# Performance work log

Hardware: AMD Instinct MI355X
Metric: run time of the kernel (lower is better)

## Reference

```python
import jax, jax.numpy as jnp
import numpy as np

B, N, D = 4, 2048, 1024
DF = 4 * D
EPS = 1e-5


def _layernorm(x, w, b):
    mu = jnp.mean(x, axis=-1, keepdims=True)
    var = jnp.mean(jnp.square(x - mu), axis=-1, keepdims=True)
    return (x - mu) * jax.lax.rsqrt(var + EPS) * w + b


def setup_inputs() -> dict:
    key = jax.random.key(0)
    ks = jax.random.split(key, 8)
    x = jax.random.normal(ks[0], (B, N, D), dtype=jnp.float32)
    # conv filter param (torch init is zeros; use small randn for numeric coverage)
    weights = jax.random.normal(ks[1], (1, 1, N), dtype=jnp.float32) * 0.02
    # registered buffer: sqrt(1/(i+1)) per token, shape (1, N, 1)
    scale = jnp.sqrt(1.0 / (jnp.arange(N, dtype=jnp.float32) + 1.0))[None, :, None]
    ln1_w = jnp.ones((D,), jnp.float32)
    ln1_b = jnp.zeros((D,), jnp.float32)
    W1 = jax.random.normal(ks[2], (DF, D), dtype=jnp.float32) * 0.02
    b1 = jnp.zeros((DF,), jnp.float32)
    W2 = jax.random.normal(ks[3], (D, DF), dtype=jnp.float32) * 0.02
    b2 = jnp.zeros((D,), jnp.float32)
    scalar = jax.random.normal(ks[4], (1,), dtype=jnp.float32) * 0.1
    ln2_w = jnp.ones((D,), jnp.float32)
    ln2_b = jnp.zeros((D,), jnp.float32)
    return dict(x=x, weights=weights, scale=scale, ln1_w=ln1_w, ln1_b=ln1_b,
                W1=W1, b1=b1, W2=W2, b2=b2, scalar=scalar, ln2_w=ln2_w, ln2_b=ln2_b)


def reference(x, weights, scale, ln1_w, ln1_b, W1, b1, W2, b2, scalar, ln2_w, ln2_b):
    n = weights.shape[-1]
    # FFT token-mixing conv: operate over token axis. x: (B,N,D) -> (B,D,N)
    xt = jnp.swapaxes(x, -2, -1)
    # real inputs -> rfft/irfft equals real(ifft(fft*fft)) from the torch code
    prod = jnp.fft.rfft(xt, n=2 * n) * jnp.fft.rfft(weights, n=2 * n)
    conv = jnp.fft.irfft(prod, n=2 * n)[..., :n]  # (B,D,N)
    x1 = jnp.swapaxes(conv, -2, -1)               # (B,N,D)
    x1 = _layernorm(x + x1 * scale, ln1_w, ln1_b)
    # GELU MLP (torch F.gelu default = exact erf gelu)
    h = jax.nn.gelu(jnp.einsum('bnd,fd->bnf', x1, W1) + b1, approximate=False)
    mlp = jnp.einsum('bnf,df->bnd', h, W2) + b2
    x2 = _layernorm(x1 + scalar * mlp, ln2_w, ln2_b)
    return x2
```

## Files before the change

### kernel.cpp

```cpp
#include <hip/hip_runtime.h>
#include <cstdint>

typedef float floatx4 __attribute__((ext_vector_type(4)));
typedef int intx8 __attribute__((ext_vector_type(8)));

__device__ __forceinline__ unsigned short f2b(float f) {
  union { float f; unsigned u; } v; v.f = f;
  return (unsigned short)((v.u + 0x7FFFu + ((v.u >> 16) & 1u)) >> 16);
}
__device__ __forceinline__ float b2f(unsigned short h) {
  union { unsigned u; float f; } v; v.u = ((unsigned)h) << 16;
  return v.f;
}

__device__ __forceinline__ void gload_lds16(const void* g, void* l) {
  __builtin_amdgcn_global_load_lds(
      (const __attribute__((address_space(1))) void*)g,
      (__attribute__((address_space(3))) void*)l, 16, 0, 0);
}


__global__ void cast_f8x64_kernel(const float* __restrict__ in,
                                  int* __restrict__ out) {
  long i = (long)blockIdx.x * 256 + threadIdx.x;
  float4 v = ((const float4*)in)[i];
  int pk = __builtin_amdgcn_cvt_pk_fp8_f32(v.x * 64.0f, v.y * 64.0f, 0, false);
  pk = __builtin_amdgcn_cvt_pk_fp8_f32(v.z * 64.0f, v.w * 64.0f, pk, true);
  out[i] = pk;
}

__global__ void build_T8_kernel(const float* __restrict__ w,
                                int* __restrict__ T8) {
  long i = (long)blockIdx.x * 256 + threadIdx.x;
  int n = (int)(i >> 9);
  int m0 = (int)(i & 511) * 4;
  float v[4];
#pragma unroll
  for (int r = 0; r < 4; ++r) {
    int m = m0 + r;
    v[r] = (m <= n) ? w[n - m] * 64.0f : 0.0f;
  }
  int pk = __builtin_amdgcn_cvt_pk_fp8_f32(v[0], v[1], 0, false);
  pk = __builtin_amdgcn_cvt_pk_fp8_f32(v[2], v[3], pk, true);
  T8[i] = pk;
}

__global__ void transpose_cast_f8_kernel(const float* __restrict__ x,
                                         unsigned char* __restrict__ xT) {
  __shared__ float tile[32][33];
  int b = blockIdx.z;
  int n0 = blockIdx.y * 32;
  int d0 = blockIdx.x * 32;
  int tx = threadIdx.x;
  int ty = threadIdx.y;
  for (int i = ty; i < 32; i += 8)
    tile[i][tx] = x[((long)b * 2048 + n0 + i) * 1024 + d0 + tx];
  __syncthreads();
  float a = tile[ty * 4 + 0][tx];
  float c = tile[ty * 4 + 1][tx];
  float e = tile[ty * 4 + 2][tx];
  float f = tile[ty * 4 + 3][tx];
  int pk = __builtin_amdgcn_cvt_pk_fp8_f32(a, c, 0, false);
  pk = __builtin_amdgcn_cvt_pk_fp8_f32(e, f, pk, true);
  *(int*)(xT + ((long)b * 1024 + d0 + tx) * 2048 + n0 + ty * 4) = pk;
}

template <int EPI, int NT, bool TRI>
__global__ __launch_bounds__(256, 4) void gemm_f8(
    const unsigned char* __restrict__ A, const unsigned char* __restrict__ B,
    int Kstride, int Kloop, long zsA, long zsB, long zsC,
    int rx, int ryb, int gxn, unsigned sclA, unsigned sclB,
    const float* __restrict__ resid, const float* __restrict__ scale,
    const float* __restrict__ bias,
    float* __restrict__ Cf, unsigned short* __restrict__ Cb,
    unsigned char* __restrict__ C8) {
  __shared__ __align__(16) unsigned char As[16 * 1040];
  __shared__ __align__(16) unsigned char Bs[16 * 1040];
  const int tid = threadIdx.x;
  const int wid = tid >> 6;
  const int lane = tid & 63;
  const int quad = lane >> 4;
  const int l16 = lane & 15;
  const int wm = (wid >> 1) * 64;
  const int wn = (wid & 1) * 64;

  const int bid = blockIdx.x;
  const int xcd = bid & 7;
  const int ib = bid >> 3;
  const int ci = ib % rx;
  const int ri = ib / rx;
  long bm, bn;
  if (TRI) {
    bm = (long)(ri == 0 ? xcd : 15 - xcd) * 128;
    bn = (long)ci * 128;
  } else {
    const int gx = xcd % gxn;
    const int gy = xcd / gxn;
    bm = (long)(gy * ryb + ri) * 128;
    bn = (long)(gx * rx + ci) * 128;
  }
  const int bz = blockIdx.z;
  const unsigned char* Ab = A + zsA * bz;
  const unsigned char* Bb = B + zsB * bz;

  floatx4 acc[4][4];
#pragma unroll
  for (int i = 0; i < 4; ++i)
#pragma unroll
    for (int j = 0; j < 4; ++j)
      acc[i][j] = floatx4{0.0f, 0.0f, 0.0f, 0.0f};

  const int srow = tid >> 3;
  const int scol = (tid & 7) * 16;
  const unsigned char* gA[4];
  const unsigned char* gB[4];
  unsigned char* lA[4];
  unsigned char* lB[4];
#pragma unroll
  for (int p = 0; p < 4; ++p) {
    gA[p] = Ab + (bm + p * 32 + srow) * (long)Kstride + scol;
    gB[p] = Bb + (bn + p * 32 + srow) * (long)Kstride + scol;
    lA[p] = As + (p * 4 + wid) * 1040;
    lB[p] = Bs + (p * 4 + wid) * 1040;
  }

  const int kend = TRI ? min(Kloop, (int)bm + 128) : Kloop;
  for (int kk = 0; kk < kend; kk += 128) {
    __syncthreads();
#pragma unroll
    for (int p = 0; p < 4; ++p) {
      gload_lds16(gA[p] + kk, lA[p]);
      gload_lds16(gB[p] + kk, lB[p]);
    }
    __syncthreads();
    intx8 af[4], bfr[4];
#pragma unroll
    for (int i = 0; i < 4; ++i) {
      const int ra = wm + i * 16 + l16;
      const int off = (ra >> 3) * 1040 + (ra & 7) * 128 + quad * 32;
      union { intx8 v; int4 q[2]; } u;
      u.q[0] = *(const int4*)(As + off);
      u.q[1] = *(const int4*)(As + off + 16);
      af[i] = u.v;
    }
#pragma unroll
    for (int j = 0; j < 4; ++j) {
      const int rb = wn + j * 16 + l16;
      const int off = (rb >> 3) * 1040 + (rb & 7) * 128 + quad * 32;
      union { intx8 v; int4 q[2]; } u;
      u.q[0] = *(const int4*)(Bs + off);
      u.q[1] = *(const int4*)(Bs + off + 16);
      bfr[j] = u.v;
    }
#pragma unroll
    for (int i = 0; i < 4; ++i)
#pragma unroll
      for (int j = 0; j < 4; ++j)
        acc[i][j] = __builtin_amdgcn_mfma_scale_f32_16x16x128_f8f6f4(
            af[i], bfr[j], acc[i][j], 0 , 0 ,
            0, sclA, 0, sclB);
  }

#pragma unroll
  for (int i = 0; i < 4; ++i)
#pragma unroll
    for (int j = 0; j < 4; ++j)
#pragma unroll
      for (int r = 0; r < 4; ++r) {
        long row = bm + wm + i * 16 + quad * 4 + r;
        long col = bn + wn + j * 16 + l16;
        long idx = (long)bz * zsC + row * (long)NT + col;
        float v = acc[i][j][r];
        if (EPI == 0) {
          Cb[idx] = f2b(v);
        } else if (EPI == 1) {
          Cf[idx] = resid[idx] + scale[row] * v;
        } else {
          v += bias[col];
          float u = v * (0.7978845608f + 0.0356774081f * v * v);
          float u2 = u * u;
          float t = __fdividef(u * (15.0f + u2), 15.0f + 6.0f * u2);
          t = fminf(fmaxf(t, -1.0f), 1.0f);
          float g = 0.5f * v * (1.0f + t);
          int pk = __builtin_amdgcn_cvt_pk_fp8_f32(g, 0.0f, 0, false);
          C8[idx] = (unsigned char)(pk & 0xFF);
        }
      }
}

__global__ __launch_bounds__(256) void ln_kernel(
    const float* __restrict__ in, const float* __restrict__ w,
    const float* __restrict__ b, unsigned short* __restrict__ outb,
    int* __restrict__ outf8) {
  const long row = blockIdx.x;
  const int tid = threadIdx.x;
  float4 v = ((const float4*)in)[row * 256 + tid];
  float s = v.x + v.y + v.z + v.w;
  float ss = v.x * v.x + v.y * v.y + v.z * v.z + v.w * v.w;
#pragma unroll
  for (int off = 32; off > 0; off >>= 1) {
    s += __shfl_down(s, off);
    ss += __shfl_down(ss, off);
  }
  __shared__ float red[8];
  const int wid = tid >> 6, lane = tid & 63;
  if (lane == 0) { red[wid] = s; red[4 + wid] = ss; }
  __syncthreads();
  s = red[0] + red[1] + red[2] + red[3];
  ss = red[4] + red[5] + red[6] + red[7];
  const float mu = s * (1.0f / 1024.0f);
  const float var = ss * (1.0f / 1024.0f) - mu * mu;
  const float rs = rsqrtf(var + 1e-5f);
  float4 wv = ((const float4*)w)[tid];
  float4 bv = ((const float4*)b)[tid];
  float o0 = (v.x - mu) * rs * wv.x + bv.x;
  float o1 = (v.y - mu) * rs * wv.y + bv.y;
  float o2 = (v.z - mu) * rs * wv.z + bv.z;
  float o3 = (v.w - mu) * rs * wv.w + bv.w;
  ushort4 u{f2b(o0), f2b(o1), f2b(o2), f2b(o3)};
  ((ushort4*)outb)[row * 256 + tid] = u;
  int pk = __builtin_amdgcn_cvt_pk_fp8_f32(o0, o1, 0, false);
  pk = __builtin_amdgcn_cvt_pk_fp8_f32(o2, o3, pk, true);
  outf8[row * 256 + tid] = pk;
}

__global__ __launch_bounds__(256) void ln2_fused_kernel(
    const unsigned short* __restrict__ y0, const unsigned short* __restrict__ y1,
    const unsigned short* __restrict__ x1b, const float* __restrict__ b2,
    const float* __restrict__ scalar_p, const float* __restrict__ w,
    const float* __restrict__ b, float* __restrict__ out) {
  const long row = blockIdx.x;
  const int tid = threadIdx.x;
  ushort4 a4 = ((const ushort4*)y0)[row * 256 + tid];
  ushort4 c4 = ((const ushort4*)y1)[row * 256 + tid];
  ushort4 xr = ((const ushort4*)x1b)[row * 256 + tid];
  float4 bias = ((const float4*)b2)[tid];
  const float scl = scalar_p[0];
  float4 v;
  v.x = b2f(xr.x) + scl * (b2f(a4.x) + b2f(c4.x) + bias.x);
  v.y = b2f(xr.y) + scl * (b2f(a4.y) + b2f(c4.y) + bias.y);
  v.z = b2f(xr.z) + scl * (b2f(a4.z) + b2f(c4.z) + bias.z);
  v.w = b2f(xr.w) + scl * (b2f(a4.w) + b2f(c4.w) + bias.w);
  float s = v.x + v.y + v.z + v.w;
  float ss = v.x * v.x + v.y * v.y + v.z * v.z + v.w * v.w;
#pragma unroll
  for (int off = 32; off > 0; off >>= 1) {
    s += __shfl_down(s, off);
    ss += __shfl_down(ss, off);
  }
  __shared__ float red[8];
  const int wid = tid >> 6, lane = tid & 63;
  if (lane == 0) { red[wid] = s; red[4 + wid] = ss; }
  __syncthreads();
  s = red[0] + red[1] + red[2] + red[3];
  ss = red[4] + red[5] + red[6] + red[7];
  const float mu = s * (1.0f / 1024.0f);
  const float var = ss * (1.0f / 1024.0f) - mu * mu;
  const float rs = rsqrtf(var + 1e-5f);
  float4 wv = ((const float4*)w)[tid];
  float4 bv = ((const float4*)b)[tid];
  float4 o;
  o.x = (v.x - mu) * rs * wv.x + bv.x;
  o.y = (v.y - mu) * rs * wv.y + bv.y;
  o.z = (v.z - mu) * rs * wv.z + bv.z;
  o.w = (v.w - mu) * rs * wv.w + bv.w;
  ((float4*)out)[row * 256 + tid] = o;
}

extern "C" void kernel_launch(void* const* d_in, const int* in_sizes, int n_in,
                              void* d_out, int out_size, void* d_ws, size_t ws_size,
                              hipStream_t stream) {
  const float* x      = (const float*)d_in[0];
  const float* wconv  = (const float*)d_in[1];
  const float* scale  = (const float*)d_in[2];
  const float* ln1w   = (const float*)d_in[3];
  const float* ln1b   = (const float*)d_in[4];
  const float* W1     = (const float*)d_in[5];
  const float* b1     = (const float*)d_in[6];
  const float* W2     = (const float*)d_in[7];
  const float* b2     = (const float*)d_in[8];
  const float* scalar = (const float*)d_in[9];
  const float* ln2w   = (const float*)d_in[10];
  const float* ln2b   = (const float*)d_in[11];
  float* out = (float*)d_out;

  const unsigned SCL_1  = 0x7F7F7F7Fu;
  const unsigned SCL_64 = 0x79797979u;

  char* ws = (char*)d_ws;
  unsigned char* xT8   = (unsigned char*)ws;  ws += (size_t)4 * 1024 * 2048;
  unsigned char* T8    = (unsigned char*)ws;  ws += (size_t)2048 * 2048;
  unsigned char* W1f8  = (unsigned char*)ws;  ws += (size_t)4096 * 1024;
  unsigned char* W2f8  = (unsigned char*)ws;  ws += (size_t)4096 * 1024;
  float* y             = (float*)ws;          ws += (size_t)8192 * 1024 * 4;
  unsigned short* yb   = (unsigned short*)ws; ws += (size_t)2 * 8192 * 1024 * 2;
  unsigned short* x1b  = (unsigned short*)ws; ws += (size_t)8192 * 1024 * 2;
  unsigned char* x1f8  = (unsigned char*)ws;  ws += (size_t)8192 * 1024;
  unsigned char* h8    = (unsigned char*)ws;  ws += (size_t)8192 * 4096;

  cast_f8x64_kernel<<<4096, 256, 0, stream>>>(W1, (int*)W1f8);
  cast_f8x64_kernel<<<4096, 256, 0, stream>>>(W2, (int*)W2f8);
  build_T8_kernel<<<4096, 256, 0, stream>>>(wconv, (int*)T8);
  transpose_cast_f8_kernel<<<dim3(32, 64, 4), dim3(32, 8), 0, stream>>>(x, xT8);

  gemm_f8<1, 1024, true><<<dim3(128, 1, 4), 256, 0, stream>>>(
      T8, xT8, 2048, 2048, 0L, (long)1024 * 2048, (long)2048 * 1024,
      8, 0, 0, SCL_64, SCL_1, x, scale, nullptr, y, nullptr, nullptr);
  ln_kernel<<<8192, 256, 0, stream>>>(y, ln1w, ln1b, x1b, (int*)x1f8);
  gemm_f8<2, 4096, false><<<dim3(2048, 1, 1), 256, 0, stream>>>(
      x1f8, W1f8, 1024, 1024, 0L, 0L, 0L,
      16, 16, 2, SCL_1, SCL_64, nullptr, nullptr, b1, nullptr, nullptr, h8);
  gemm_f8<0, 1024, false><<<dim3(512, 1, 2), 256, 0, stream>>>(
      h8, W2f8, 4096, 2048, 2048L, 2048L, (long)8192 * 1024,
      8, 8, 1, SCL_1, SCL_64, nullptr, nullptr, nullptr, nullptr, yb, nullptr);
  ln2_fused_kernel<<<8192, 256, 0, stream>>>(
      yb, yb + (size_t)8192 * 1024, x1b, b2, scalar, ln2w, ln2b, out);
}
```

Measured before the change: 286.7 us.

## Stage GEMM epilogue through LDS for coalesced vector stores; move conv residual into LN1

The GEMM epilogue now writes accumulators into shared memory (with a rotation swizzle) in two half-tile passes, then each thread reads a contiguous row segment and issues 16-byte vectorized stores of fp8 or bf16. This replaces scattered per-element byte/short stores. The token-conv GEMM now stores a bf16 result instead of an fp32 residual-plus-scale result, and the residual add with the scale moves into the LN1 kernel, halving the intermediate traffic. In exchange it adds extra barriers and LDS round-trips, and bf16 rounding of the conv output before the residual add.

```diff
diff --git a/kernel.cpp b/kernel.cpp
--- a/kernel.cpp
+++ b/kernel.cpp
@@ -65,17 +65,16 @@
   *(int*)(xT + ((long)b * 1024 + d0 + tx) * 2048 + n0 + ty * 4) = pk;
 }
 
-template <int EPI, int NT, bool TRI>
+template <bool GELU, bool TRI>
 __global__ __launch_bounds__(256, 4) void gemm_f8(
     const unsigned char* __restrict__ A, const unsigned char* __restrict__ B,
-    int Kstride, int Kloop, long zsA, long zsB, long zsC,
+    int NT, int Kstride, int Kloop, long zsA, long zsB, long zsC,
     int rx, int ryb, int gxn, unsigned sclA, unsigned sclB,
-    const float* __restrict__ resid, const float* __restrict__ scale,
     const float* __restrict__ bias,
-    float* __restrict__ Cf, unsigned short* __restrict__ Cb,
-    unsigned char* __restrict__ C8) {
-  __shared__ __align__(16) unsigned char As[16 * 1040];
-  __shared__ __align__(16) unsigned char Bs[16 * 1040];
+    unsigned short* __restrict__ Cb, unsigned char* __restrict__ C8) {
+  __shared__ __align__(16) unsigned char smem[2 * 16 * 1040];
+  unsigned char* As = smem;
+  unsigned char* Bs = smem + 16 * 1040;
   const int tid = threadIdx.x;
   const int wid = tid >> 6;
   const int lane = tid & 63;
@@ -161,40 +160,95 @@
             0, sclA, 0, sclB);
   }
 
-#pragma unroll
-  for (int i = 0; i < 4; ++i)
-#pragma unroll
-    for (int j = 0; j < 4; ++j)
-#pragma unroll
-      for (int r = 0; r < 4; ++r) {
-        long row = bm + wm + i * 16 + quad * 4 + r;
-        long col = bn + wn + j * 16 + l16;
-        long idx = (long)bz * zsC + row * (long)NT + col;
-        float v = acc[i][j][r];
-        if (EPI == 0) {
-          Cb[idx] = f2b(v);
-        } else if (EPI == 1) {
-          Cf[idx] = resid[idx] + scale[row] * v;
-        } else {
-          v += bias[col];
-          float u = v * (0.7978845608f + 0.0356774081f * v * v);
-          float u2 = u * u;
-          float t = __fdividef(u * (15.0f + u2), 15.0f + 6.0f * u2);
-          t = fminf(fmaxf(t, -1.0f), 1.0f);
-          float g = 0.5f * v * (1.0f + t);
-          int pk = __builtin_amdgcn_cvt_pk_fp8_f32(g, 0.0f, 0, false);
-          C8[idx] = (unsigned char)(pk & 0xFF);
+  float bj[4];
+  if (GELU) {
+#pragma unroll
+    for (int j = 0; j < 4; ++j) bj[j] = bias[bn + wn + j * 16 + l16];
+  }
+  float* cbuf = (float*)smem;
+  const int rl_r = tid >> 2;
+  const int seg = tid & 3;
+#pragma unroll
+  for (int p = 0; p < 2; ++p) {
+    __syncthreads();
+    if ((wid >> 1) == p) {
+#pragma unroll
+      for (int i = 0; i < 4; ++i)
+#pragma unroll
+        for (int j = 0; j < 4; ++j)
+#pragma unroll
+          for (int r = 0; r < 4; ++r) {
+            const int rl = i * 16 + quad * 4 + r;
+            const int col = wn + j * 16 + l16;
+            float v = acc[i][j][r];
+            if (GELU) {
+              v += bj[j];
+              float u = v * (0.7978845608f + 0.0356774081f * v * v);
+              float u2 = u * u;
+              float t = __fdividef(u * (15.0f + u2), 15.0f + 6.0f * u2);
+              t = fminf(fmaxf(t, -1.0f), 1.0f);
+              v = 0.5f * v * (1.0f + t);
+            }
+            cbuf[rl * 128 + ((col + rl * 4) & 127)] = v;
+          }
+    }
+    __syncthreads();
+    float4 f[8];
+#pragma unroll
+    for (int k = 0; k < 8; ++k) {
+      const int g = (seg * 8 + k + rl_r) & 31;
+      f[k] = *(const float4*)(cbuf + rl_r * 128 + g * 4);
+    }
+    const long grow = bm + p * 64 + rl_r;
+    if (GELU) {
+      int4 o[2];
+#pragma unroll
+      for (int s = 0; s < 2; ++s) {
+        int d[4];
+#pragma unroll
+        for (int q = 0; q < 4; ++q) {
+          float4 x4 = f[s * 4 + q];
+          int pk = __builtin_amdgcn_cvt_pk_fp8_f32(x4.x, x4.y, 0, false);
+          pk = __builtin_amdgcn_cvt_pk_fp8_f32(x4.z, x4.w, pk, true);
+          d[q] = pk;
         }
+        o[s] = int4{d[0], d[1], d[2], d[3]};
       }
-}
-
-__global__ __launch_bounds__(256) void ln_kernel(
-    const float* __restrict__ in, const float* __restrict__ w,
+      int4* dst = (int4*)(C8 + (long)bz * zsC + grow * (long)NT + bn + seg * 32);
+      dst[0] = o[0];
+      dst[1] = o[1];
+    } else {
+      int4* dst = (int4*)(Cb + (long)bz * zsC + grow * (long)NT + bn + seg * 32);
+#pragma unroll
+      for (int s = 0; s < 4; ++s) {
+        float4 a4 = f[s * 2];
+        float4 c4 = f[s * 2 + 1];
+        int d0 = (unsigned)f2b(a4.x) | ((unsigned)f2b(a4.y) << 16);
+        int d1 = (unsigned)f2b(a4.z) | ((unsigned)f2b(a4.w) << 16);
+        int d2 = (unsigned)f2b(c4.x) | ((unsigned)f2b(c4.y) << 16);
+        int d3 = (unsigned)f2b(c4.z) | ((unsigned)f2b(c4.w) << 16);
+        dst[s] = int4{d0, d1, d2, d3};
+      }
+    }
+  }
+}
+
+__global__ __launch_bounds__(256) void ln1_kernel(
+    const unsigned short* __restrict__ conv, const float* __restrict__ x,
+    const float* __restrict__ scale, const float* __restrict__ w,
     const float* __restrict__ b, unsigned short* __restrict__ outb,
     int* __restrict__ outf8) {
   const long row = blockIdx.x;
+  const int n = (int)(row & 2047);
   const int tid = threadIdx.x;
-  float4 v = ((const float4*)in)[row * 256 + tid];
+  float4 xv = ((const float4*)x)[row * 256 + tid];
+  ushort4 cv = ((const ushort4*)conv)[row * 256 + tid];
+  const float sc = scale[n];
+  float4 v;
+  v.x = xv.x + sc * b2f(cv.x);
+  v.y = xv.y + sc * b2f(cv.y);
+  v.z = xv.z + sc * b2f(cv.z);
+  v.w = xv.w + sc * b2f(cv.w);
   float s = v.x + v.y + v.z + v.w;
   float ss = v.x * v.x + v.y * v.y + v.z * v.z + v.w * v.w;
 #pragma unroll
@@ -292,7 +346,7 @@
   unsigned char* T8    = (unsigned char*)ws;  ws += (size_t)2048 * 2048;
   unsigned char* W1f8  = (unsigned char*)ws;  ws += (size_t)4096 * 1024;
   unsigned char* W2f8  = (unsigned char*)ws;  ws += (size_t)4096 * 1024;
-  float* y             = (float*)ws;          ws += (size_t)8192 * 1024 * 4;
+  unsigned short* convb= (unsigned short*)ws; ws += (size_t)8192 * 1024 * 2;
   unsigned short* yb   = (unsigned short*)ws; ws += (size_t)2 * 8192 * 1024 * 2;
   unsigned short* x1b  = (unsigned short*)ws; ws += (size_t)8192 * 1024 * 2;
   unsigned char* x1f8  = (unsigned char*)ws;  ws += (size_t)8192 * 1024;
@@ -303,16 +357,16 @@
   build_T8_kernel<<<4096, 256, 0, stream>>>(wconv, (int*)T8);
   transpose_cast_f8_kernel<<<dim3(32, 64, 4), dim3(32, 8), 0, stream>>>(x, xT8);
 
-  gemm_f8<1, 1024, true><<<dim3(128, 1, 4), 256, 0, stream>>>(
-      T8, xT8, 2048, 2048, 0L, (long)1024 * 2048, (long)2048 * 1024,
-      8, 0, 0, SCL_64, SCL_1, x, scale, nullptr, y, nullptr, nullptr);
-  ln_kernel<<<8192, 256, 0, stream>>>(y, ln1w, ln1b, x1b, (int*)x1f8);
-  gemm_f8<2, 4096, false><<<dim3(2048, 1, 1), 256, 0, stream>>>(
-      x1f8, W1f8, 1024, 1024, 0L, 0L, 0L,
-      16, 16, 2, SCL_1, SCL_64, nullptr, nullptr, b1, nullptr, nullptr, h8);
-  gemm_f8<0, 1024, false><<<dim3(512, 1, 2), 256, 0, stream>>>(
-      h8, W2f8, 4096, 2048, 2048L, 2048L, (long)8192 * 1024,
-      8, 8, 1, SCL_1, SCL_64, nullptr, nullptr, nullptr, nullptr, yb, nullptr);
+  gemm_f8<false, true><<<dim3(128, 1, 4), 256, 0, stream>>>(
+      T8, xT8, 1024, 2048, 2048, 0L, (long)1024 * 2048, (long)2048 * 1024,
+      8, 0, 0, SCL_64, SCL_1, nullptr, convb, nullptr);
+  ln1_kernel<<<8192, 256, 0, stream>>>(convb, x, scale, ln1w, ln1b, x1b, (int*)x1f8);
+  gemm_f8<true, false><<<dim3(2048, 1, 1), 256, 0, stream>>>(
+      x1f8, W1f8, 4096, 1024, 1024, 0L, 0L, 0L,
+      16, 16, 2, SCL_1, SCL_64, b1, nullptr, h8);
+  gemm_f8<false, false><<<dim3(512, 1, 2), 256, 0, stream>>>(
+      h8, W2f8, 1024, 4096, 2048, 2048L, 2048L, (long)8192 * 1024,
+      8, 8, 1, SCL_1, SCL_64, nullptr, yb, nullptr);
   ln2_fused_kernel<<<8192, 256, 0, stream>>>(
       yb, yb + (size_t)8192 * 1024, x1b, b2, scalar, ln2w, ln2b, out);
 }
```

Result: slower. 318.4 us (+11.1%).
